# Optimization experiments

Hardware: AMD Instinct MI355X
Metric: run time of the kernel (lower is better)

The kernel has to match this reference:

```python
import jax, jax.numpy as jnp
import numpy as np

CLAMP = 15  # relative positions clipped to [-15, 15], shifted to [0, 30]


def setup_inputs() -> dict:
    key = jax.random.key(0)
    ks = jax.random.split(key, 8)
    B, L, C, P = 2, 512, 256, 128
    return {
        "single_repr": jax.random.normal(ks[0], (B, L, C), jnp.float32),
        "pair_bias": jax.random.normal(ks[1], (B, L, L, 2), jnp.float32),
        "mask": jax.random.uniform(ks[2], (B, L), jnp.float32),
        "w_outer": jax.random.normal(ks[3], (C * C, P), jnp.float32) * (1.0 / C),
        "b_outer": jax.random.normal(ks[4], (P,), jnp.float32) * 0.02,
        "pos_embed": jax.random.normal(ks[5], (32, P), jnp.float32) * 0.02,
        "w_bias": jax.random.normal(ks[6], (2, P), jnp.float32) * 0.02,
        "b_bias": jax.random.normal(ks[7], (P,), jnp.float32) * 0.02,
    }


def reference(single_repr, pair_bias, mask, w_outer, b_outer, pos_embed, w_bias, b_bias):
    B, L, C = single_repr.shape
    P = w_outer.shape[-1]
    # Fused outer-product + projection: z[b,i,j,p] = sum_{c,d} s[b,i,c] s[b,j,d] W[c,d,p]
    # done as two matmuls, never materializing the [B,L,L,C,C] tensor.
    W = w_outer.reshape(C, C, P)
    tmp = jnp.einsum('bjd,cdp->bjcp', single_repr, W)          # [B,L,C,P]
    z = jnp.einsum('bic,bjcp->bijp', single_repr, tmp) + b_outer  # [B,L,L,P]
    # pair bias projection (pair_bias_dim=2 != pair_dim -> project)
    z = z + (pair_bias @ w_bias + b_bias)
    # relative-position embedding
    pos = jnp.arange(L)
    rel_pos = jnp.clip(pos[:, None] - pos[None, :], -CLAMP, CLAMP) + CLAMP  # [L,L] in [0,30]
    z = z + pos_embed[rel_pos]
    # pair mask
    pair_mask = mask[:, :, None] * mask[:, None, :]
    z = z * pair_mask[..., None]
    return z
```

## Files before the change

### kernel.cpp

```cpp
#include <hip/hip_runtime.h>
#include <stdint.h>

#define GLOBAL_AS __attribute__((address_space(1)))
#define LDS_AS    __attribute__((address_space(3)))

typedef __attribute__((ext_vector_type(8))) short short8;
typedef __attribute__((ext_vector_type(4))) float f32x4;
typedef __attribute__((ext_vector_type(4))) float float4v;
typedef __attribute__((ext_vector_type(2))) float float2v;
typedef __attribute__((ext_vector_type(4))) unsigned short ushort4v;

static constexpr int Bc = 2;
static constexpr int Lc = 512;
static constexpr int Cc = 256;
static constexpr int Pc = 128;
static constexpr int NP = Pc * Cc;
static constexpr size_t TMPB = (size_t)Lc * NP;

__device__ __forceinline__ unsigned short f2bf(float x) {
  unsigned int u = __builtin_bit_cast(unsigned int, x);
  u += 0x7FFFu + ((u >> 16) & 1u);
  return (unsigned short)(u >> 16);
}

__device__ __forceinline__ void gload_lds16(const void* g, void* l) {
  __builtin_amdgcn_global_load_lds((const GLOBAL_AS unsigned int*)g,
                                   (LDS_AS unsigned int*)l, 16, 0, 0);
}

__global__ void convert_s_kernel(const float* __restrict__ s,
                                 unsigned short* __restrict__ out) {
  const int idx = (blockIdx.x * 256 + threadIdx.x) * 4;
  float4v v = *(const float4v*)&s[idx];
  ushort4v o;
  #pragma unroll
  for (int i = 0; i < 4; ++i) o[i] = f2bf(v[i]);
  *(ushort4v*)&out[idx] = o;
}

__global__ void prep_w_kernel(const float* __restrict__ w,
                              unsigned short* __restrict__ wT) {
  __shared__ unsigned short lds[128 * 258];
  const int c = blockIdx.x;
  const int t = threadIdx.x;
  const float* wc = w + (size_t)c * (Cc * Pc);
  #pragma unroll 4
  for (int it = 0; it < 128; ++it) {
    const int idx = it * 256 + t;
    const int d = idx >> 7, p = idx & 127;
    lds[p * 258 + d] = f2bf(wc[idx]);
  }
  __syncthreads();
  unsigned short* o = wT + (size_t)c * NP;
  #pragma unroll 4
  for (int it = 0; it < 128; ++it) {
    const int idx = it * 256 + t;
    const int p = idx >> 8, d = idx & 255;
    o[idx] = lds[p * 258 + d];
  }
}

__global__ __launch_bounds__(256) void gemm1_swapped_kernel(
    const unsigned short* __restrict__ sbf,
    const unsigned short* __restrict__ wT,
    unsigned short* __restrict__ tmpT,
    int b_base) {
  __shared__ unsigned short Ws[128 * 64];
  __shared__ unsigned short Ss[128 * 64];
  const int tid = threadIdx.x;
  const int wave = tid >> 6, lane = tid & 63;
  const int z = blockIdx.z;
  const int b = b_base + z;
  const int n0 = blockIdx.x * 128;
  const int j0 = blockIdx.y * 128;
  const int p_wg = n0 >> 8;
  const int c_base = n0 & 255;
  const unsigned short* sB = sbf + b * Lc * Cc;
  unsigned short* tT = tmpT + (size_t)z * TMPB;

  const int wr = wave >> 1, wcn = wave & 1;
  const int lr = lane & 15, lk = (lane >> 4) << 3;

  f32x4 acc[4][4];
  const f32x4 zero = {0.f, 0.f, 0.f, 0.f};
  #pragma unroll
  for (int m = 0; m < 4; ++m)
    #pragma unroll
    for (int n = 0; n < 4; ++n) acc[m][n] = zero;

  #pragma unroll 1
  for (int kt = 0; kt < 4; ++kt) {
    const int d0 = kt * 64;
    __syncthreads();
    #pragma unroll
    for (int op = 0; op < 4; ++op) {
      const int idx = op * 256 + tid;
      const int row = idx >> 3, col = (idx & 7) << 3;
      gload_lds16(&wT[(size_t)((c_base + row) * 128 + p_wg) * 256 + d0 + col],
                  &Ws[(size_t)(op * 256 + wave * 64) * 8]);
    }
    #pragma unroll
    for (int op = 0; op < 4; ++op) {
      const int idx = op * 256 + tid;
      const int row = idx >> 3, col = (idx & 7) << 3;
      gload_lds16(&sB[(j0 + row) * Cc + d0 + col],
                  &Ss[(size_t)(op * 256 + wave * 64) * 8]);
    }
    __syncthreads();
    #pragma unroll
    for (int kk = 0; kk < 2; ++kk) {
      short8 aw[4], bs[4];
      #pragma unroll
      for (int m = 0; m < 4; ++m)
        aw[m] = *(const short8*)&Ws[(wr * 64 + m * 16 + lr) * 64 + kk * 32 + lk];
      #pragma unroll
      for (int n = 0; n < 4; ++n)
        bs[n] = *(const short8*)&Ss[(wcn * 64 + n * 16 + lr) * 64 + kk * 32 + lk];
      #pragma unroll
      for (int m = 0; m < 4; ++m)
        #pragma unroll
        for (int n = 0; n < 4; ++n)
          acc[m][n] = __builtin_amdgcn_mfma_f32_16x16x32_bf16(aw[m], bs[n], acc[m][n], 0, 0, 0);
    }
  }

  const int rbase = wr * 64 + ((lane >> 4) << 2);
  #pragma unroll
  for (int n = 0; n < 4; ++n) {
    const int j = j0 + wcn * 64 + n * 16 + lr;
    unsigned short* dst = &tT[(size_t)j * NP + n0 + rbase];
    #pragma unroll
    for (int m = 0; m < 4; ++m) {
      ushort4v o;
      #pragma unroll
      for (int q = 0; q < 4; ++q) o[q] = f2bf(acc[m][n][q]);
      *(ushort4v*)&dst[m * 16] = o;
    }
  }
}

__global__ __launch_bounds__(256) void gemm2_swapped_kernel(
    const unsigned short* __restrict__ sbf,
    const unsigned short* __restrict__ tmpT,
    const float* __restrict__ pair_bias,
    const float* __restrict__ mask,
    const float* __restrict__ b_outer,
    const float* __restrict__ pos_embed,
    const float* __restrict__ w_bias,
    const float* __restrict__ b_bias,
    float* __restrict__ out,
    int b_base) {
  __shared__ unsigned short Ts[128 * 64];
  __shared__ unsigned short Ss[128 * 64];
  const int tid = threadIdx.x;
  const int wave = tid >> 6, lane = tid & 63;
  const int z = blockIdx.z;
  const int b = b_base + z;
  const int j = blockIdx.x;
  const int i0 = blockIdx.y * 128;
  const unsigned short* sB = sbf + b * Lc * Cc;
  const unsigned short* tB = tmpT + (size_t)z * TMPB + (size_t)j * NP;

  const int wr = wave >> 1, wcn = wave & 1;
  const int lr = lane & 15, lk = (lane >> 4) << 3;

  f32x4 acc[4][4];
  const f32x4 zero = {0.f, 0.f, 0.f, 0.f};
  #pragma unroll
  for (int m = 0; m < 4; ++m)
    #pragma unroll
    for (int n = 0; n < 4; ++n) acc[m][n] = zero;

  #pragma unroll 1
  for (int kt = 0; kt < 4; ++kt) {
    const int c0 = kt * 64;
    __syncthreads();
    #pragma unroll
    for (int op = 0; op < 4; ++op) {
      const int idx = op * 256 + tid;
      const int row = idx >> 3, col = (idx & 7) << 3;
      gload_lds16(&tB[row * 256 + c0 + col],
                  &Ts[(size_t)(op * 256 + wave * 64) * 8]);
    }
    #pragma unroll
    for (int op = 0; op < 4; ++op) {
      const int idx = op * 256 + tid;
      const int row = idx >> 3, col = (idx & 7) << 3;
      gload_lds16(&sB[(i0 + row) * Cc + c0 + col],
                  &Ss[(size_t)(op * 256 + wave * 64) * 8]);
    }
    __syncthreads();
    #pragma unroll
    for (int kk = 0; kk < 2; ++kk) {
      short8 at[4], bi[4];
      #pragma unroll
      for (int m = 0; m < 4; ++m)
        at[m] = *(const short8*)&Ts[(wr * 64 + m * 16 + lr) * 64 + kk * 32 + lk];
      #pragma unroll
      for (int n = 0; n < 4; ++n)
        bi[n] = *(const short8*)&Ss[(wcn * 64 + n * 16 + lr) * 64 + kk * 32 + lk];
      #pragma unroll
      for (int m = 0; m < 4; ++m)
        #pragma unroll
        for (int n = 0; n < 4; ++n)
          acc[m][n] = __builtin_amdgcn_mfma_f32_16x16x32_bf16(at[m], bi[n], acc[m][n], 0, 0, 0);
    }
  }

  const int pbase = wr * 64 + ((lane >> 4) << 2);
  const float mj = mask[b * Lc + j];

  float4v bsum[4], wb0[4], wb1[4];
  #pragma unroll
  for (int m = 0; m < 4; ++m) {
    const int p = pbase + m * 16;
    bsum[m] = *(const float4v*)&b_outer[p] + *(const float4v*)&b_bias[p];
    wb0[m] = *(const float4v*)&w_bias[p];
    wb1[m] = *(const float4v*)&w_bias[Pc + p];
  }

  #pragma unroll
  for (int n = 0; n < 4; ++n) {
    const int i = i0 + wcn * 64 + n * 16 + lr;
    const float sc = mask[b * Lc + i] * mj;
    const size_t rowoff = (size_t)(b * Lc + i) * Lc + j;
    const float2v pb = *(const float2v*)&pair_bias[rowoff * 2];
    int rel = i - j;
    rel = rel < -15 ? -15 : (rel > 15 ? 15 : rel);
    rel += 15;
    const float* pe_row = pos_embed + rel * Pc;
    float* drow = out + rowoff * Pc;
    #pragma unroll
    for (int m = 0; m < 4; ++m) {
      const int p = pbase + m * 16;
      const float4v pe4 = *(const float4v*)&pe_row[p];
      float4v v = acc[m][n] + bsum[m] + pb[0] * wb0[m] + pb[1] * wb1[m] + pe4;
      *(float4v*)&drow[p] = v * sc;
    }
  }
}

extern "C" void kernel_launch(void* const* d_in, const int* in_sizes, int n_in,
                              void* d_out, int out_size, void* d_ws, size_t ws_size,
                              hipStream_t stream) {
  const float* s         = (const float*)d_in[0];
  const float* pair_bias = (const float*)d_in[1];
  const float* mask      = (const float*)d_in[2];
  const float* w_outer   = (const float*)d_in[3];
  const float* b_outer   = (const float*)d_in[4];
  const float* pos_embed = (const float*)d_in[5];
  const float* w_bias    = (const float*)d_in[6];
  const float* b_bias    = (const float*)d_in[7];
  float* out = (float*)d_out;

  unsigned char* ws = (unsigned char*)d_ws;
  unsigned short* s_bf = (unsigned short*)ws;
  unsigned short* wT   = (unsigned short*)(ws + (512u << 10));
  unsigned short* tmpT = (unsigned short*)(ws + (512u << 10) + (16u << 20));

  const size_t need_batched = (512u << 10) + (16u << 20) + 2 * (TMPB * 2);
  const bool batched = ws_size >= need_batched;

  convert_s_kernel<<<256, 256, 0, stream>>>(s, s_bf);
  prep_w_kernel<<<256, 256, 0, stream>>>(w_outer, wT);

  if (batched) {
    gemm1_swapped_kernel<<<dim3(256, 4, 2), 256, 0, stream>>>(s_bf, wT, tmpT, 0);
    gemm2_swapped_kernel<<<dim3(512, 4, 2), 256, 0, stream>>>(
        s_bf, tmpT, pair_bias, mask, b_outer, pos_embed, w_bias, b_bias, out, 0);
  } else {
    for (int b = 0; b < Bc; ++b) {
      gemm1_swapped_kernel<<<dim3(256, 4, 1), 256, 0, stream>>>(s_bf, wT, tmpT, b);
      gemm2_swapped_kernel<<<dim3(512, 4, 1), 256, 0, stream>>>(
          s_bf, tmpT, pair_bias, mask, b_outer, pos_embed, w_bias, b_bias, out, b);
    }
  }
}
```

Before: 438.1 us.

## Use 256x256 double-buffered GEMM tiles with 512 threads and reorganised weight layout

Both GEMMs move to a shared 256x256-tile routine run by 512-thread blocks, with double-buffered LDS staging so the next K slice loads while MFMAs run on the current one. The weight is re-laid out per output channel p so each block reads one contiguous 256x256 slab. In gemm2 one block now covers two j rows (one per wave row). The aim is more reuse per loaded byte and load/compute overlap. The cost is 128 KB of LDS and more accumulator registers per block, which may reduce occupancy, and the small-workspace fallback path is gone.

```diff
diff --git a/kernel.cpp b/kernel.cpp
--- a/kernel.cpp
+++ b/kernel.cpp
@@ -39,7 +39,7 @@
 }
 
 __global__ void prep_w_kernel(const float* __restrict__ w,
-                              unsigned short* __restrict__ wT) {
+                              unsigned short* __restrict__ wA) {
   __shared__ unsigned short lds[128 * 258];
   const int c = blockIdx.x;
   const int t = threadIdx.x;
@@ -51,86 +51,99 @@
     lds[p * 258 + d] = f2bf(wc[idx]);
   }
   __syncthreads();
-  unsigned short* o = wT + (size_t)c * NP;
   #pragma unroll 4
   for (int it = 0; it < 128; ++it) {
     const int idx = it * 256 + t;
     const int p = idx >> 8, d = idx & 255;
-    o[idx] = lds[p * 258 + d];
-  }
-}
-
-__global__ __launch_bounds__(256) void gemm1_swapped_kernel(
+    wA[(size_t)p * 65536 + (size_t)c * 256 + d] = lds[p * 258 + d];
+  }
+}
+
+__device__ __forceinline__ void run_gemm_k256(
+    const unsigned short* __restrict__ gA,
+    const unsigned short* __restrict__ gB,
+    unsigned short (&As)[2][256 * 64],
+    unsigned short (&Bs)[2][256 * 64],
+    const int tid, const int wave, const int wr, const int wc,
+    const int lr, const int lk,
+    f32x4 (&acc)[8][4]) {
+  auto stage = [&](int sel, int t) {
+    const int k0 = t * 64;
+    #pragma unroll
+    for (int r = 0; r < 4; ++r) {
+      const int idx = r * 512 + tid;
+      const int row = idx >> 3, col = (idx & 7) << 3;
+      gload_lds16(&gA[(size_t)row * 256 + k0 + col],
+                  &As[sel][(size_t)(r * 512 + wave * 64) * 8]);
+    }
+    #pragma unroll
+    for (int r = 0; r < 4; ++r) {
+      const int idx = r * 512 + tid;
+      const int row = idx >> 3, col = (idx & 7) << 3;
+      gload_lds16(&gB[(size_t)row * 256 + k0 + col],
+                  &Bs[sel][(size_t)(r * 512 + wave * 64) * 8]);
+    }
+  };
+
+  stage(0, 0);
+  __syncthreads();
+  #pragma unroll
+  for (int t = 0; t < 4; ++t) {
+    const int cur = t & 1;
+    if (t < 3) stage(cur ^ 1, t + 1);
+    #pragma unroll
+    for (int kk = 0; kk < 2; ++kk) {
+      short8 a[8], b[4];
+      #pragma unroll
+      for (int m = 0; m < 8; ++m)
+        a[m] = *(const short8*)&As[cur][(wr * 128 + m * 16 + lr) * 64 + kk * 32 + lk];
+      #pragma unroll
+      for (int n = 0; n < 4; ++n)
+        b[n] = *(const short8*)&Bs[cur][(wc * 64 + n * 16 + lr) * 64 + kk * 32 + lk];
+      #pragma unroll
+      for (int m = 0; m < 8; ++m)
+        #pragma unroll
+        for (int n = 0; n < 4; ++n)
+          acc[m][n] = __builtin_amdgcn_mfma_f32_16x16x32_bf16(a[m], b[n], acc[m][n], 0, 0, 0);
+    }
+    __syncthreads();
+  }
+}
+
+__global__ __launch_bounds__(512, 2) void gemm1_k(
     const unsigned short* __restrict__ sbf,
-    const unsigned short* __restrict__ wT,
-    unsigned short* __restrict__ tmpT,
-    int b_base) {
-  __shared__ unsigned short Ws[128 * 64];
-  __shared__ unsigned short Ss[128 * 64];
+    const unsigned short* __restrict__ wA,
+    unsigned short* __restrict__ tmpT) {
+  __shared__ unsigned short As[2][256 * 64];
+  __shared__ unsigned short Bs[2][256 * 64];
   const int tid = threadIdx.x;
   const int wave = tid >> 6, lane = tid & 63;
+  const int wr = wave >> 2, wc = wave & 3;
+  const int lr = lane & 15, lk = (lane >> 4) << 3;
+  const int p = blockIdx.x;
+  const int j0 = blockIdx.y * 256;
   const int z = blockIdx.z;
-  const int b = b_base + z;
-  const int n0 = blockIdx.x * 128;
-  const int j0 = blockIdx.y * 128;
-  const int p_wg = n0 >> 8;
-  const int c_base = n0 & 255;
-  const unsigned short* sB = sbf + b * Lc * Cc;
+
+  const unsigned short* gA = wA + (size_t)p * 65536;
+  const unsigned short* gB = sbf + (size_t)z * Lc * Cc + (size_t)j0 * 256;
+
+  f32x4 acc[8][4];
+  const f32x4 zero = {0.f, 0.f, 0.f, 0.f};
+  #pragma unroll
+  for (int m = 0; m < 8; ++m)
+    #pragma unroll
+    for (int n = 0; n < 4; ++n) acc[m][n] = zero;
+
+  run_gemm_k256(gA, gB, As, Bs, tid, wave, wr, wc, lr, lk, acc);
+
   unsigned short* tT = tmpT + (size_t)z * TMPB;
-
-  const int wr = wave >> 1, wcn = wave & 1;
-  const int lr = lane & 15, lk = (lane >> 4) << 3;
-
-  f32x4 acc[4][4];
-  const f32x4 zero = {0.f, 0.f, 0.f, 0.f};
-  #pragma unroll
-  for (int m = 0; m < 4; ++m)
-    #pragma unroll
-    for (int n = 0; n < 4; ++n) acc[m][n] = zero;
-
-  #pragma unroll 1
-  for (int kt = 0; kt < 4; ++kt) {
-    const int d0 = kt * 64;
-    __syncthreads();
-    #pragma unroll
-    for (int op = 0; op < 4; ++op) {
-      const int idx = op * 256 + tid;
-      const int row = idx >> 3, col = (idx & 7) << 3;
-      gload_lds16(&wT[(size_t)((c_base + row) * 128 + p_wg) * 256 + d0 + col],
-                  &Ws[(size_t)(op * 256 + wave * 64) * 8]);
-    }
-    #pragma unroll
-    for (int op = 0; op < 4; ++op) {
-      const int idx = op * 256 + tid;
-      const int row = idx >> 3, col = (idx & 7) << 3;
-      gload_lds16(&sB[(j0 + row) * Cc + d0 + col],
-                  &Ss[(size_t)(op * 256 + wave * 64) * 8]);
-    }
-    __syncthreads();
-    #pragma unroll
-    for (int kk = 0; kk < 2; ++kk) {
-      short8 aw[4], bs[4];
-      #pragma unroll
-      for (int m = 0; m < 4; ++m)
-        aw[m] = *(const short8*)&Ws[(wr * 64 + m * 16 + lr) * 64 + kk * 32 + lk];
-      #pragma unroll
-      for (int n = 0; n < 4; ++n)
-        bs[n] = *(const short8*)&Ss[(wcn * 64 + n * 16 + lr) * 64 + kk * 32 + lk];
-      #pragma unroll
-      for (int m = 0; m < 4; ++m)
-        #pragma unroll
-        for (int n = 0; n < 4; ++n)
-          acc[m][n] = __builtin_amdgcn_mfma_f32_16x16x32_bf16(aw[m], bs[n], acc[m][n], 0, 0, 0);
-    }
-  }
-
-  const int rbase = wr * 64 + ((lane >> 4) << 2);
+  const int cq = wr * 128 + ((lane >> 4) << 2);
   #pragma unroll
   for (int n = 0; n < 4; ++n) {
-    const int j = j0 + wcn * 64 + n * 16 + lr;
-    unsigned short* dst = &tT[(size_t)j * NP + n0 + rbase];
-    #pragma unroll
-    for (int m = 0; m < 4; ++m) {
+    const int j = j0 + wc * 64 + n * 16 + lr;
+    unsigned short* dst = tT + (size_t)j * NP + p * 256 + cq;
+    #pragma unroll
+    for (int m = 0; m < 8; ++m) {
       ushort4v o;
       #pragma unroll
       for (int q = 0; q < 4; ++q) o[q] = f2bf(acc[m][n][q]);
@@ -139,7 +152,7 @@
   }
 }
 
-__global__ __launch_bounds__(256) void gemm2_swapped_kernel(
+__global__ __launch_bounds__(512, 2) void gemm2_k(
     const unsigned short* __restrict__ sbf,
     const unsigned short* __restrict__ tmpT,
     const float* __restrict__ pair_bias,
@@ -148,82 +161,45 @@
     const float* __restrict__ pos_embed,
     const float* __restrict__ w_bias,
     const float* __restrict__ b_bias,
-    float* __restrict__ out,
-    int b_base) {
-  __shared__ unsigned short Ts[128 * 64];
-  __shared__ unsigned short Ss[128 * 64];
+    float* __restrict__ out) {
+  __shared__ unsigned short As[2][256 * 64];
+  __shared__ unsigned short Bs[2][256 * 64];
   const int tid = threadIdx.x;
   const int wave = tid >> 6, lane = tid & 63;
+  const int wr = wave >> 2, wc = wave & 3;
+  const int lr = lane & 15, lk = (lane >> 4) << 3;
+  const int jt = blockIdx.x;
+  const int i0 = blockIdx.y * 256;
   const int z = blockIdx.z;
-  const int b = b_base + z;
-  const int j = blockIdx.x;
-  const int i0 = blockIdx.y * 128;
-  const unsigned short* sB = sbf + b * Lc * Cc;
-  const unsigned short* tB = tmpT + (size_t)z * TMPB + (size_t)j * NP;
-
-  const int wr = wave >> 1, wcn = wave & 1;
-  const int lr = lane & 15, lk = (lane >> 4) << 3;
-
-  f32x4 acc[4][4];
+
+  const unsigned short* gA = tmpT + (size_t)z * TMPB + (size_t)jt * 65536;
+  const unsigned short* gB = sbf + (size_t)z * Lc * Cc + (size_t)i0 * 256;
+
+  f32x4 acc[8][4];
   const f32x4 zero = {0.f, 0.f, 0.f, 0.f};
   #pragma unroll
-  for (int m = 0; m < 4; ++m)
+  for (int m = 0; m < 8; ++m)
     #pragma unroll
     for (int n = 0; n < 4; ++n) acc[m][n] = zero;
 
-  #pragma unroll 1
-  for (int kt = 0; kt < 4; ++kt) {
-    const int c0 = kt * 64;
-    __syncthreads();
-    #pragma unroll
-    for (int op = 0; op < 4; ++op) {
-      const int idx = op * 256 + tid;
-      const int row = idx >> 3, col = (idx & 7) << 3;
-      gload_lds16(&tB[row * 256 + c0 + col],
-                  &Ts[(size_t)(op * 256 + wave * 64) * 8]);
-    }
-    #pragma unroll
-    for (int op = 0; op < 4; ++op) {
-      const int idx = op * 256 + tid;
-      const int row = idx >> 3, col = (idx & 7) << 3;
-      gload_lds16(&sB[(i0 + row) * Cc + c0 + col],
-                  &Ss[(size_t)(op * 256 + wave * 64) * 8]);
-    }
-    __syncthreads();
-    #pragma unroll
-    for (int kk = 0; kk < 2; ++kk) {
-      short8 at[4], bi[4];
-      #pragma unroll
-      for (int m = 0; m < 4; ++m)
-        at[m] = *(const short8*)&Ts[(wr * 64 + m * 16 + lr) * 64 + kk * 32 + lk];
-      #pragma unroll
-      for (int n = 0; n < 4; ++n)
-        bi[n] = *(const short8*)&Ss[(wcn * 64 + n * 16 + lr) * 64 + kk * 32 + lk];
-      #pragma unroll
-      for (int m = 0; m < 4; ++m)
-        #pragma unroll
-        for (int n = 0; n < 4; ++n)
-          acc[m][n] = __builtin_amdgcn_mfma_f32_16x16x32_bf16(at[m], bi[n], acc[m][n], 0, 0, 0);
-    }
-  }
-
-  const int pbase = wr * 64 + ((lane >> 4) << 2);
-  const float mj = mask[b * Lc + j];
-
-  float4v bsum[4], wb0[4], wb1[4];
-  #pragma unroll
-  for (int m = 0; m < 4; ++m) {
-    const int p = pbase + m * 16;
-    bsum[m] = *(const float4v*)&b_outer[p] + *(const float4v*)&b_bias[p];
-    wb0[m] = *(const float4v*)&w_bias[p];
-    wb1[m] = *(const float4v*)&w_bias[Pc + p];
+  run_gemm_k256(gA, gB, As, Bs, tid, wave, wr, wc, lr, lk, acc);
+
+  const int j = jt * 2 + wr;
+  const int pq = (lane >> 4) << 2;
+  const float mj = mask[z * Lc + j];
+
+  float4v base8[8];
+  #pragma unroll
+  for (int m = 0; m < 8; ++m) {
+    const int pp = m * 16 + pq;
+    base8[m] = *(const float4v*)&b_outer[pp] + *(const float4v*)&b_bias[pp];
   }
 
   #pragma unroll
   for (int n = 0; n < 4; ++n) {
-    const int i = i0 + wcn * 64 + n * 16 + lr;
-    const float sc = mask[b * Lc + i] * mj;
-    const size_t rowoff = (size_t)(b * Lc + i) * Lc + j;
+    const int i = i0 + wc * 64 + n * 16 + lr;
+    const float sc = mask[z * Lc + i] * mj;
+    const size_t rowoff = ((size_t)(z * Lc + i)) * Lc + j;
     const float2v pb = *(const float2v*)&pair_bias[rowoff * 2];
     int rel = i - j;
     rel = rel < -15 ? -15 : (rel > 15 ? 15 : rel);
@@ -231,11 +207,13 @@
     const float* pe_row = pos_embed + rel * Pc;
     float* drow = out + rowoff * Pc;
     #pragma unroll
-    for (int m = 0; m < 4; ++m) {
-      const int p = pbase + m * 16;
-      const float4v pe4 = *(const float4v*)&pe_row[p];
-      float4v v = acc[m][n] + bsum[m] + pb[0] * wb0[m] + pb[1] * wb1[m] + pe4;
-      *(float4v*)&drow[p] = v * sc;
+    for (int m = 0; m < 8; ++m) {
+      const int pp = m * 16 + pq;
+      const float4v wb0 = *(const float4v*)&w_bias[pp];
+      const float4v wb1 = *(const float4v*)&w_bias[Pc + pp];
+      const float4v pe4 = *(const float4v*)&pe_row[pp];
+      float4v v = acc[m][n] + base8[m] + pb[0] * wb0 + pb[1] * wb1 + pe4;
+      *(float4v*)&drow[pp] = v * sc;
     }
   }
 }
@@ -255,24 +233,13 @@
 
   unsigned char* ws = (unsigned char*)d_ws;
   unsigned short* s_bf = (unsigned short*)ws;
-  unsigned short* wT   = (unsigned short*)(ws + (512u << 10));
+  unsigned short* wA   = (unsigned short*)(ws + (512u << 10));
   unsigned short* tmpT = (unsigned short*)(ws + (512u << 10) + (16u << 20));
 
-  const size_t need_batched = (512u << 10) + (16u << 20) + 2 * (TMPB * 2);
-  const bool batched = ws_size >= need_batched;
-
   convert_s_kernel<<<256, 256, 0, stream>>>(s, s_bf);
-  prep_w_kernel<<<256, 256, 0, stream>>>(w_outer, wT);
-
-  if (batched) {
-    gemm1_swapped_kernel<<<dim3(256, 4, 2), 256, 0, stream>>>(s_bf, wT, tmpT, 0);
-    gemm2_swapped_kernel<<<dim3(512, 4, 2), 256, 0, stream>>>(
-        s_bf, tmpT, pair_bias, mask, b_outer, pos_embed, w_bias, b_bias, out, 0);
-  } else {
-    for (int b = 0; b < Bc; ++b) {
-      gemm1_swapped_kernel<<<dim3(256, 4, 1), 256, 0, stream>>>(s_bf, wT, tmpT, b);
-      gemm2_swapped_kernel<<<dim3(512, 4, 1), 256, 0, stream>>>(
-          s_bf, tmpT, pair_bias, mask, b_outer, pos_embed, w_bias, b_bias, out, b);
-    }
-  }
-}
+  prep_w_kernel<<<256, 256, 0, stream>>>(w_outer, wA);
+  gemm1_k<<<dim3(128, 2, 2), 512, 0, stream>>>(s_bf, wA, tmpT);
+  gemm2_k<<<dim3(256, 2, 2), 512, 0, stream>>>(s_bf, tmpT, pair_bias, mask,
+                                               b_outer, pos_embed, w_bias,
+                                               b_bias, out);
+}
```

Result: faster. 427.6 us (-2.4%).
